# Kernel optimization log

Measured on AMD Instinct MI355X. Metric: run time of the kernel, lower is better.

The kernel has to match this reference:

```python
import jax, jax.numpy as jnp
import numpy as np

B_, N, C, H = 2048, 49, 384, 12
WH, WW = 7, 7
HEAD_DIM = C // H
SCALE = HEAD_DIM ** -0.5
TABLE = (2 * WH - 1) * (2 * WW - 1)  # 169


def _relative_position_index():
    coords = np.stack(np.meshgrid(np.arange(WH), np.arange(WW), indexing='ij'))  # [2,Wh,Ww]
    flat = coords.reshape(2, -1)  # [2,N]
    rel = flat[:, :, None] - flat[:, None, :]  # [2,N,N]
    rel = rel.transpose(1, 2, 0).astype(np.int32)  # [N,N,2]
    rel[:, :, 0] += WH - 1
    rel[:, :, 1] += WW - 1
    rel[:, :, 0] *= 2 * WW - 1
    return rel.sum(-1)  # [N,N] int32 in [0,169)


def setup_inputs() -> dict:
    key = jax.random.key(0)
    ks = jax.random.split(key, 8)
    return {
        'x': jax.random.normal(ks[0], (B_, N, C), jnp.float32),
        'mask': jax.random.normal(ks[1], (B_, 1, N, N), jnp.float32),
        'stagein': jax.random.uniform(ks[2], (B_, N, C), jnp.float32),
        'rel_bias_table': jax.random.normal(ks[3], (TABLE, H), jnp.float32) * 0.02,
        'rel_pos_index': jnp.asarray(_relative_position_index()),
        'qkv_w': jax.random.normal(ks[4], (3 * C, C), jnp.float32) * 0.02,
        'qkv_b': jax.random.normal(ks[5], (3 * C,), jnp.float32) * 0.02,
        'proj_w': jax.random.normal(ks[6], (C, C), jnp.float32) * 0.02,
        'proj_b': jax.random.normal(ks[7], (C,), jnp.float32) * 0.02,
    }


def reference(x, mask, stagein, rel_bias_table, rel_pos_index, qkv_w, qkv_b, proj_w, proj_b):
    x = x * stagein  # stagein is not None branch
    qkv = x @ qkv_w.T + qkv_b  # [B_, N, 3C]
    qkv = qkv.reshape(B_, N, 3, H, HEAD_DIM).transpose(2, 0, 3, 1, 4)  # [3,B_,H,N,hd]
    q, k, v = qkv[0], qkv[1], qkv[2]
    q = q * SCALE
    attn = jnp.einsum('bhnd,bhmd->bhnm', q, k)  # [B_,H,N,N]
    # relative position bias gather: [N*N] -> [N,N,H] -> [1,H,N,N]
    bias = rel_bias_table[rel_pos_index.reshape(-1)].reshape(N, N, H)
    bias = bias.transpose(2, 0, 1)[None]
    attn = jax.nn.softmax(attn + bias + mask, axis=-1)
    out = jnp.einsum('bhnm,bhmd->bhnd', attn, v)  # [B_,H,N,hd]
    out = out.transpose(0, 2, 1, 3).reshape(B_, N, C)
    return out @ proj_w.T + proj_b
```

## Files before the change

### kernel.cpp

```cpp
#include <hip/hip_runtime.h>
#include <hip/hip_bf16.h>
#include <stdint.h>

#define NWIN 2048
#define NTOK 49
#define CDIM 384
#define NHEAD 12
#define HD 32
#define C3 1152
#define NN2 2401
#define MROWS 100352

typedef __bf16 bf16x8 __attribute__((ext_vector_type(8)));
typedef float f32x4 __attribute__((ext_vector_type(4)));
typedef uint32_t u32x4 __attribute__((ext_vector_type(4)));
typedef unsigned int u32;

static __device__ __forceinline__ unsigned short f2bf(float f) {
  uint32_t u = __builtin_bit_cast(uint32_t, f);
  u += 0x7fffu + ((u >> 16) & 1u);
  return (unsigned short)(u >> 16);
}

static __device__ __forceinline__ u32 pk2(float a, float b) {
  return (u32)f2bf(a) | ((u32)f2bf(b) << 16);
}

static __device__ __forceinline__ void gload_lds16(const void* g, void* l) {
  __builtin_amdgcn_global_load_lds((const __attribute__((address_space(1))) void*)g,
                                   (__attribute__((address_space(3))) void*)l,
                                   16, 0, 0);
}

static __device__ __forceinline__ bf16x8 zero8() {
  u32x4 z = {0u, 0u, 0u, 0u};
  return __builtin_bit_cast(bf16x8, z);
}

__global__ void prep_kernel(const float* __restrict__ qkv_w, const float* __restrict__ proj_w,
                            const float* __restrict__ table, const int* __restrict__ idx,
                            unsigned short* __restrict__ wq, unsigned short* __restrict__ wp,
                            float* __restrict__ biasT) {
  const int NW1 = C3 * CDIM;
  const int NW2 = CDIM * CDIM;
  const int NB = NHEAD * NN2;
  int i = blockIdx.x * blockDim.x + threadIdx.x;
  int stride = gridDim.x * blockDim.x;
  for (int t = i; t < NW1 + NW2 + NB; t += stride) {
    if (t < NW1) {
      wq[t] = f2bf(qkv_w[t]);
    } else if (t < NW1 + NW2) {
      int j = t - NW1;
      wp[j] = f2bf(proj_w[j]);
    } else {
      int j = t - NW1 - NW2;
      int h = j / NN2;
      int nm = j - h * NN2;
      int m = nm / 49, n = nm - m * 49;
      biasT[j] = table[idx[n * 49 + m] * NHEAD + h];
    }
  }
}

__global__ void maskT_kernel(const float* __restrict__ mask, float* __restrict__ maskT) {
  __shared__ float t[NN2];
  const int b = blockIdx.x;
  for (int i = threadIdx.x; i < NN2; i += 256) t[i] = mask[(size_t)b * NN2 + i];
  __syncthreads();
  for (int i = threadIdx.x; i < NN2; i += 256) {
    int m = i / 49, n = i - m * 49;
    maskT[(size_t)b * NN2 + i] = t[n * 49 + m];
  }
}

__global__ void mul_kernel(const float4* __restrict__ x, const float4* __restrict__ s,
                           u32x4* __restrict__ A, int n8) {
  int i0 = blockIdx.x * blockDim.x + threadIdx.x;
  int stride = gridDim.x * blockDim.x;
  for (int t = i0; t < n8; t += stride) {
    float4 a0 = x[2 * t], a1 = x[2 * t + 1];
    float4 b0 = s[2 * t], b1 = s[2 * t + 1];
    union { unsigned short us[8]; u32x4 v; } o;
    o.us[0] = f2bf(a0.x * b0.x); o.us[1] = f2bf(a0.y * b0.y);
    o.us[2] = f2bf(a0.z * b0.z); o.us[3] = f2bf(a0.w * b0.w);
    o.us[4] = f2bf(a1.x * b1.x); o.us[5] = f2bf(a1.y * b1.y);
    o.us[6] = f2bf(a1.z * b1.z); o.us[7] = f2bf(a1.w * b1.w);
    A[t] = o.v;
  }
}

__launch_bounds__(256, 2)
__global__ void qkv_gemm(const unsigned short* __restrict__ A,
                         const unsigned short* __restrict__ Bw,
                         const float* __restrict__ qkvb,
                         unsigned short* __restrict__ qo,
                         unsigned short* __restrict__ ko,
                         unsigned short* __restrict__ vo) {
  __shared__ unsigned short As[128 * 64];
  __shared__ unsigned short Bs[128 * 64];
  const int tid = threadIdx.x;
  const int w = tid >> 6, l = tid & 63;
  const int l15 = l & 15, lhi = l >> 4;
  const int wgid = (blockIdx.x & 7) * 882 + (blockIdx.x >> 3);
  const int mt = wgid / 9, nt = wgid - mt * 9;
  const int wr = w >> 1, wc = w & 1;
  const int srow = tid >> 3;
  const int scb = (tid & 7) ^ (srow & 7);
  const unsigned short* Ag = A + (size_t)(mt * 128 + srow) * CDIM + scb * 8;
  const unsigned short* Bg = Bw + (size_t)(nt * 128 + srow) * CDIM + scb * 8;
  unsigned short* Asl = As + srow * 64 + (tid & 7) * 8;
  unsigned short* Bsl = Bs + srow * 64 + (tid & 7) * 8;
  const f32x4 z4 = {0.f, 0.f, 0.f, 0.f};
  f32x4 acc[4][4];
#pragma unroll
  for (int m = 0; m < 4; ++m)
#pragma unroll
    for (int n = 0; n < 4; ++n) acc[m][n] = z4;
  const int xr = l15 & 7;
  for (int kt = 0; kt < 6; ++kt) {
    const unsigned short* ag = Ag + kt * 64;
    const unsigned short* bg = Bg + kt * 64;
#pragma unroll
    for (int i = 0; i < 4; ++i) {
      gload_lds16(ag + i * 32 * CDIM, Asl + i * 2048);
      gload_lds16(bg + i * 32 * CDIM, Bsl + i * 2048);
    }
    __syncthreads();
#pragma unroll
    for (int kk = 0; kk < 2; ++kk) {
      const int sl = ((kk << 2) | lhi) ^ xr;
      bf16x8 af[4], bfr[4];
#pragma unroll
      for (int m = 0; m < 4; ++m)
        af[m] = *(const bf16x8*)(As + (wr * 64 + m * 16 + l15) * 64 + sl * 8);
#pragma unroll
      for (int n = 0; n < 4; ++n)
        bfr[n] = *(const bf16x8*)(Bs + (wc * 64 + n * 16 + l15) * 64 + sl * 8);
#pragma unroll
      for (int m = 0; m < 4; ++m)
#pragma unroll
        for (int n = 0; n < 4; ++n)
          acc[m][n] = __builtin_amdgcn_mfma_f32_16x16x32_bf16(af[m], bfr[n], acc[m][n], 0, 0, 0);
    }
    __syncthreads();
  }
  const float SCALE_F = 0.17677669529663687f;
  const int six = nt * 2 + wc;
  const int which = six / 6;
  const int cbase = (six - which * 6) * 64;
  unsigned short* outw = (which == 0) ? qo : ((which == 1) ? ko : vo);
  const float* bptr = qkvb + which * CDIM;
#pragma unroll
  for (int m = 0; m < 4; ++m) {
#pragma unroll
    for (int j = 0; j < 4; ++j) {
      const int r = mt * 128 + wr * 64 + m * 16 + lhi * 4 + j;
      const int bwin = r / 49;
      const int ntok = r - bwin * 49;
#pragma unroll
      for (int n = 0; n < 4; ++n) {
        const int c = cbase + n * 16 + l15;
        const int h = c >> 5, d = c & 31;
        float val = acc[m][n][j] + bptr[c];
        if (which == 0) val *= SCALE_F;
        outw[(((size_t)bwin * NHEAD + h) * NTOK + ntok) * HD + d] = f2bf(val);
      }
    }
  }
}

__launch_bounds__(256, 2)
__global__ void attn_kernel(const unsigned short* __restrict__ q,
                            const unsigned short* __restrict__ kmat,
                            const unsigned short* __restrict__ vmat,
                            const float* __restrict__ maskT,
                            const float* __restrict__ biasT,
                            unsigned short* __restrict__ attnout) {
  __shared__ unsigned short vT_lds[4][32 * 72];
  const int tid = threadIdx.x;
  const int w = tid >> 6, l = tid & 63;
  const int l15 = l & 15, lhi = l >> 4;
  const int wg = (blockIdx.x & 7) * 768 + (blockIdx.x >> 3);
  const int b = wg / 3, it = wg - b * 3;
  unsigned short* Vw = &vT_lds[w][0];
  const float* maskb = maskT + (size_t)b * NN2;
  const f32x4 z4 = {0.f, 0.f, 0.f, 0.f};
  const int h = it * 4 + w;
  const size_t hb = ((size_t)b * NHEAD + h) * NTOK * HD;
  const unsigned short* qb = q + hb;
  const unsigned short* kb = kmat + hb;
  const unsigned short* vb = vmat + hb;
  {
    const int n = l;
    unsigned short tmp[32];
    if (n < 49) {
      *(u32x4*)(&tmp[0])  = *(const u32x4*)(vb + n * 32);
      *(u32x4*)(&tmp[8])  = *(const u32x4*)(vb + n * 32 + 8);
      *(u32x4*)(&tmp[16]) = *(const u32x4*)(vb + n * 32 + 16);
      *(u32x4*)(&tmp[24]) = *(const u32x4*)(vb + n * 32 + 24);
    } else {
#pragma unroll
      for (int d2 = 0; d2 < 32; ++d2) tmp[d2] = 0;
    }
#pragma unroll
    for (int d2 = 0; d2 < 32; ++d2) Vw[d2 * 72 + n] = tmp[d2];
  }
  bf16x8 aq[4], bk[4];
#pragma unroll
  for (int t = 0; t < 4; ++t) {
    const int row = t * 16 + l15;
    if (row < 49) {
      aq[t] = *(const bf16x8*)(qb + row * 32 + lhi * 8);
      bk[t] = *(const bf16x8*)(kb + row * 32 + lhi * 8);
    } else {
      aq[t] = zero8();
      bk[t] = zero8();
    }
  }
  const float* biash = biasT + h * NN2;
  u32 P4[4][4][2];
#pragma unroll
  for (int nt = 0; nt < 4; ++nt) {
    f32x4 s4[4];
#pragma unroll
    for (int mt = 0; mt < 4; ++mt)
      s4[mt] = __builtin_amdgcn_mfma_f32_16x16x32_bf16(bk[mt], aq[nt], z4, 0, 0, 0);
    const int n = nt * 16 + l15;
#pragma unroll
    for (int mt = 0; mt < 4; ++mt) {
#pragma unroll
      for (int r = 0; r < 4; ++r) {
        const int m = mt * 16 + lhi * 4 + r;
        float val = -1e30f;
        if (n < 49 && m < 49)
          val = s4[mt][r] + biash[m * 49 + n] + maskb[m * 49 + n];
        s4[mt][r] = val;
      }
    }
    float mx = s4[0][0];
#pragma unroll
    for (int mt = 0; mt < 4; ++mt)
#pragma unroll
      for (int r = 0; r < 4; ++r) mx = fmaxf(mx, s4[mt][r]);
    mx = fmaxf(mx, __shfl_xor(mx, 16));
    mx = fmaxf(mx, __shfl_xor(mx, 32));
    float sum = 0.f;
#pragma unroll
    for (int mt = 0; mt < 4; ++mt)
#pragma unroll
      for (int r = 0; r < 4; ++r) {
        s4[mt][r] = __expf(s4[mt][r] - mx);
        sum += s4[mt][r];
      }
    sum += __shfl_xor(sum, 16);
    sum += __shfl_xor(sum, 32);
    const float rinv = 1.0f / sum;
#pragma unroll
    for (int mt = 0; mt < 4; ++mt) {
      P4[nt][mt][0] = pk2(s4[mt][0] * rinv, s4[mt][1] * rinv);
      P4[nt][mt][1] = pk2(s4[mt][2] * rinv, s4[mt][3] * rinv);
    }
  }
  const int sA = ((l >> 4) & 1) * 32 + l15;
  const int sB = sA + 16;
  const bool hi_sel = (l & 32) != 0;
  f32x4 o[4][2];
#pragma unroll
  for (int ti = 0; ti < 4; ++ti) { o[ti][0] = z4; o[ti][1] = z4; }
#pragma unroll
  for (int kk = 0; kk < 2; ++kk) {
    bf16x8 bv0 = *(const bf16x8*)(Vw + l15 * 72 + kk * 32 + lhi * 8);
    bf16x8 bv1 = *(const bf16x8*)(Vw + (16 + l15) * 72 + kk * 32 + lhi * 8);
#pragma unroll
    for (int ti = 0; ti < 4; ++ti) {
      int x0 = __shfl((int)P4[ti][2 * kk][0], sA);
      int x1 = __shfl((int)P4[ti][2 * kk][1], sA);
      int y0 = __shfl((int)P4[ti][2 * kk + 1][0], sA);
      int y1 = __shfl((int)P4[ti][2 * kk + 1][1], sA);
      int x2 = __shfl((int)P4[ti][2 * kk][0], sB);
      int x3 = __shfl((int)P4[ti][2 * kk][1], sB);
      int y2 = __shfl((int)P4[ti][2 * kk + 1][0], sB);
      int y3 = __shfl((int)P4[ti][2 * kk + 1][1], sB);
      u32x4 f;
      f[0] = (u32)(hi_sel ? y0 : x0);
      f[1] = (u32)(hi_sel ? y1 : x1);
      f[2] = (u32)(hi_sel ? y2 : x2);
      f[3] = (u32)(hi_sel ? y3 : x3);
      bf16x8 pa = __builtin_bit_cast(bf16x8, f);
      o[ti][0] = __builtin_amdgcn_mfma_f32_16x16x32_bf16(pa, bv0, o[ti][0], 0, 0, 0);
      o[ti][1] = __builtin_amdgcn_mfma_f32_16x16x32_bf16(pa, bv1, o[ti][1], 0, 0, 0);
    }
  }
#pragma unroll
  for (int ti = 0; ti < 4; ++ti) {
#pragma unroll
    for (int r = 0; r < 4; ++r) {
      const int n = ti * 16 + lhi * 4 + r;
      if (n < 49) {
        unsigned short* orow = attnout + ((size_t)b * NTOK + n) * CDIM + h * HD;
        orow[l15] = f2bf(o[ti][0][r]);
        orow[16 + l15] = f2bf(o[ti][1][r]);
      }
    }
  }
}

__launch_bounds__(256, 2)
__global__ void proj_gemm(const unsigned short* __restrict__ A,
                          const unsigned short* __restrict__ Bw,
                          const float* __restrict__ pb,
                          float* __restrict__ out) {
  __shared__ unsigned short As[128 * 64];
  __shared__ unsigned short Bs[128 * 64];
  const int tid = threadIdx.x;
  const int w = tid >> 6, l = tid & 63;
  const int l15 = l & 15, lhi = l >> 4;
  const int wgid = (blockIdx.x & 7) * 294 + (blockIdx.x >> 3);
  const int mt = wgid / 3, nt = wgid - mt * 3;
  const int wr = w >> 1, wc = w & 1;
  const int srow = tid >> 3;
  const int scb = (tid & 7) ^ (srow & 7);
  const unsigned short* Ag = A + (size_t)(mt * 128 + srow) * CDIM + scb * 8;
  const unsigned short* Bg = Bw + (size_t)(nt * 128 + srow) * CDIM + scb * 8;
  unsigned short* Asl = As + srow * 64 + (tid & 7) * 8;
  unsigned short* Bsl = Bs + srow * 64 + (tid & 7) * 8;
  const f32x4 z4 = {0.f, 0.f, 0.f, 0.f};
  f32x4 acc[4][4];
#pragma unroll
  for (int m = 0; m < 4; ++m)
#pragma unroll
    for (int n = 0; n < 4; ++n) acc[m][n] = z4;
  const int xr = l15 & 7;
  for (int kt = 0; kt < 6; ++kt) {
    const unsigned short* ag = Ag + kt * 64;
    const unsigned short* bg = Bg + kt * 64;
#pragma unroll
    for (int i = 0; i < 4; ++i) {
      gload_lds16(ag + i * 32 * CDIM, Asl + i * 2048);
      gload_lds16(bg + i * 32 * CDIM, Bsl + i * 2048);
    }
    __syncthreads();
#pragma unroll
    for (int kk = 0; kk < 2; ++kk) {
      const int sl = ((kk << 2) | lhi) ^ xr;
      bf16x8 af[4], bfr[4];
#pragma unroll
      for (int m = 0; m < 4; ++m)
        af[m] = *(const bf16x8*)(As + (wr * 64 + m * 16 + l15) * 64 + sl * 8);
#pragma unroll
      for (int n = 0; n < 4; ++n)
        bfr[n] = *(const bf16x8*)(Bs + (wc * 64 + n * 16 + l15) * 64 + sl * 8);
#pragma unroll
      for (int m = 0; m < 4; ++m)
#pragma unroll
        for (int n = 0; n < 4; ++n)
          acc[m][n] = __builtin_amdgcn_mfma_f32_16x16x32_bf16(af[m], bfr[n], acc[m][n], 0, 0, 0);
    }
    __syncthreads();
  }
#pragma unroll
  for (int m = 0; m < 4; ++m) {
#pragma unroll
    for (int j = 0; j < 4; ++j) {
      const int r = mt * 128 + wr * 64 + m * 16 + lhi * 4 + j;
      float* orow = out + (size_t)r * CDIM;
#pragma unroll
      for (int n = 0; n < 4; ++n) {
        const int c = nt * 128 + wc * 64 + n * 16 + l15;
        orow[c] = acc[m][n][j] + pb[c];
      }
    }
  }
}

extern "C" void kernel_launch(void* const* d_in, const int* in_sizes, int n_in,
                              void* d_out, int out_size, void* d_ws, size_t ws_size,
                              hipStream_t stream) {
  const float* x       = (const float*)d_in[0];
  const float* mask    = (const float*)d_in[1];
  const float* stagein = (const float*)d_in[2];
  const float* table   = (const float*)d_in[3];
  const int*   idx     = (const int*)d_in[4];
  const float* qkv_w   = (const float*)d_in[5];
  const float* qkv_b   = (const float*)d_in[6];
  const float* proj_w  = (const float*)d_in[7];
  const float* proj_b  = (const float*)d_in[8];
  float* out = (float*)d_out;
  char* ws = (char*)d_ws;

  const size_t SZA = (size_t)MROWS * CDIM * 2;
  unsigned short* Abf = (unsigned short*)(ws);
  unsigned short* qb  = (unsigned short*)(ws + SZA);
  unsigned short* kb  = (unsigned short*)(ws + 2 * SZA);
  unsigned short* vb  = (unsigned short*)(ws + 3 * SZA);
  unsigned short* wq  = (unsigned short*)(ws + 4 * SZA);
  unsigned short* wp  = (unsigned short*)(ws + 4 * SZA + (size_t)C3 * CDIM * 2);
  float* biasT        = (float*)(ws + 4 * SZA + (size_t)C3 * CDIM * 2 + (size_t)CDIM * CDIM * 2);
  float* maskT        = biasT + (size_t)NHEAD * NN2;
  unsigned short* attnout = Abf;

  prep_kernel<<<dim3(512), dim3(256), 0, stream>>>(qkv_w, proj_w, table, idx, wq, wp, biasT);
  maskT_kernel<<<dim3(NWIN), dim3(256), 0, stream>>>(mask, maskT);
  mul_kernel<<<dim3(2048), dim3(256), 0, stream>>>((const float4*)x, (const float4*)stagein,
                                                   (u32x4*)Abf, MROWS * CDIM / 8);
  qkv_gemm<<<dim3(784 * 9), dim3(256), 0, stream>>>(Abf, wq, qkv_b, qb, kb, vb);
  attn_kernel<<<dim3(NWIN * 3), dim3(256), 0, stream>>>(qb, kb, vb, maskT, biasT, attnout);
  proj_gemm<<<dim3(784 * 3), dim3(256), 0, stream>>>(attnout, wp, proj_b, out);
}
```

Measured before the change: 422.0 us.

## Store Q/K/V token-major and raise GEMM occupancy bounds

The QKV GEMM epilogue now writes q, k and v as row-major [tokens, 384] arrays instead of scattering them into a per-head [B,H,N,hd] layout, and it hoists the bias loads out of the row loop. The attention kernel now reads each head's slice with a 384-element stride. This removes the per-element divide by 49 and the scattered stores from the epilogue, but the attention loads become strided. Both GEMMs also raise their launch bounds from 2 to 4 blocks per SM, which may limit registers and cause spills.

Result: slower. 458.3 us (+8.6%).

```diff
diff --git a/kernel.cpp b/kernel.cpp
--- a/kernel.cpp
+++ b/kernel.cpp
@@ -89,7 +89,7 @@
   }
 }
 
-__launch_bounds__(256, 2)
+__launch_bounds__(256, 4)
 __global__ void qkv_gemm(const unsigned short* __restrict__ A,
                          const unsigned short* __restrict__ Bw,
                          const float* __restrict__ qkvb,
@@ -150,20 +150,20 @@
   const int cbase = (six - which * 6) * 64;
   unsigned short* outw = (which == 0) ? qo : ((which == 1) ? ko : vo);
   const float* bptr = qkvb + which * CDIM;
+  float bv4[4];
+#pragma unroll
+  for (int n = 0; n < 4; ++n) bv4[n] = bptr[cbase + n * 16 + l15];
 #pragma unroll
   for (int m = 0; m < 4; ++m) {
+    const int r0 = mt * 128 + wr * 64 + m * 16 + lhi * 4;
 #pragma unroll
     for (int j = 0; j < 4; ++j) {
-      const int r = mt * 128 + wr * 64 + m * 16 + lhi * 4 + j;
-      const int bwin = r / 49;
-      const int ntok = r - bwin * 49;
+      unsigned short* orow = outw + (size_t)(r0 + j) * CDIM;
 #pragma unroll
       for (int n = 0; n < 4; ++n) {
-        const int c = cbase + n * 16 + l15;
-        const int h = c >> 5, d = c & 31;
-        float val = acc[m][n][j] + bptr[c];
+        float val = acc[m][n][j] + bv4[n];
         if (which == 0) val *= SCALE_F;
-        outw[(((size_t)bwin * NHEAD + h) * NTOK + ntok) * HD + d] = f2bf(val);
+        orow[cbase + n * 16 + l15] = f2bf(val);
       }
     }
   }
@@ -186,18 +186,18 @@
   const float* maskb = maskT + (size_t)b * NN2;
   const f32x4 z4 = {0.f, 0.f, 0.f, 0.f};
   const int h = it * 4 + w;
-  const size_t hb = ((size_t)b * NHEAD + h) * NTOK * HD;
-  const unsigned short* qb = q + hb;
-  const unsigned short* kb = kmat + hb;
-  const unsigned short* vb = vmat + hb;
+  const size_t rowbase = (size_t)b * NTOK * CDIM + h * HD;
+  const unsigned short* qb = q + rowbase;
+  const unsigned short* kb = kmat + rowbase;
+  const unsigned short* vb = vmat + rowbase;
   {
     const int n = l;
     unsigned short tmp[32];
     if (n < 49) {
-      *(u32x4*)(&tmp[0])  = *(const u32x4*)(vb + n * 32);
-      *(u32x4*)(&tmp[8])  = *(const u32x4*)(vb + n * 32 + 8);
-      *(u32x4*)(&tmp[16]) = *(const u32x4*)(vb + n * 32 + 16);
-      *(u32x4*)(&tmp[24]) = *(const u32x4*)(vb + n * 32 + 24);
+      *(u32x4*)(&tmp[0])  = *(const u32x4*)(vb + (size_t)n * CDIM);
+      *(u32x4*)(&tmp[8])  = *(const u32x4*)(vb + (size_t)n * CDIM + 8);
+      *(u32x4*)(&tmp[16]) = *(const u32x4*)(vb + (size_t)n * CDIM + 16);
+      *(u32x4*)(&tmp[24]) = *(const u32x4*)(vb + (size_t)n * CDIM + 24);
     } else {
 #pragma unroll
       for (int d2 = 0; d2 < 32; ++d2) tmp[d2] = 0;
@@ -210,8 +210,8 @@
   for (int t = 0; t < 4; ++t) {
     const int row = t * 16 + l15;
     if (row < 49) {
-      aq[t] = *(const bf16x8*)(qb + row * 32 + lhi * 8);
-      bk[t] = *(const bf16x8*)(kb + row * 32 + lhi * 8);
+      aq[t] = *(const bf16x8*)(qb + (size_t)row * CDIM + lhi * 8);
+      bk[t] = *(const bf16x8*)(kb + (size_t)row * CDIM + lhi * 8);
     } else {
       aq[t] = zero8();
       bk[t] = zero8();
@@ -305,7 +305,7 @@
   }
 }
 
-__launch_bounds__(256, 2)
+__launch_bounds__(256, 4)
 __global__ void proj_gemm(const unsigned short* __restrict__ A,
                           const unsigned short* __restrict__ Bw,
                           const float* __restrict__ pb,
```
